# Performance work log

Hardware: AMD Instinct MI355X
Metric: run time of the kernel (lower is better)

## Reference

```python
import jax, jax.numpy as jnp
import numpy as np

N_NODES = 100000
N_EDGES = 600000
D_IN = 128
D_HID = 128
N_CLASSES = 64


def setup_inputs() -> dict:
    key = jax.random.key(0)
    ks = jax.random.split(key, 8)
    x = jax.random.normal(ks[0], (N_NODES, D_IN), dtype=jnp.float32)
    src = jax.random.randint(ks[1], (N_EDGES,), 0, N_NODES, dtype=jnp.int32)
    dst = jax.random.randint(ks[2], (N_EDGES,), 0, N_NODES, dtype=jnp.int32)
    s = 1.0 / np.sqrt(D_IN)
    W_self1 = jax.random.normal(ks[3], (D_IN, D_HID), dtype=jnp.float32) * s
    W_neigh1 = jax.random.normal(ks[4], (D_IN, D_HID), dtype=jnp.float32) * s
    b1 = jnp.zeros((D_HID,), dtype=jnp.float32)
    s2 = 1.0 / np.sqrt(D_HID)
    W_self2 = jax.random.normal(ks[5], (D_HID, N_CLASSES), dtype=jnp.float32) * s2
    W_neigh2 = jax.random.normal(ks[6], (D_HID, N_CLASSES), dtype=jnp.float32) * s2
    b2 = jnp.zeros((N_CLASSES,), dtype=jnp.float32)
    return {"x": x, "src": src, "dst": dst,
            "W_self1": W_self1, "W_neigh1": W_neigh1, "b1": b1,
            "W_self2": W_self2, "W_neigh2": W_neigh2, "b2": b2}


def _sage_conv(h, src, dst, W_self, W_neigh, b):
    # mean aggregation over in-neighbors (DGL SAGEConv 'mean')
    n = h.shape[0]
    nbr_sum = jax.ops.segment_sum(h[src], dst, num_segments=n)  # [N, d]
    deg = jax.ops.segment_sum(jnp.ones(src.shape, h.dtype), dst, num_segments=n)
    nbr_mean = nbr_sum / jnp.maximum(deg, 1.0)[:, None]
    return h @ W_self + nbr_mean @ W_neigh + b


def reference(x, src, dst, W_self1, W_neigh1, b1, W_self2, W_neigh2, b2):
    # dropout is identity in eval mode
    h = _sage_conv(x, src, dst, W_self1, W_neigh1, b1)
    h = jax.nn.relu(h)
    h = _sage_conv(h, src, dst, W_self2, W_neigh2, b2)
    return h
```

## Files before the change

### kernel.cpp

```cpp
#include <hip/hip_runtime.h>

#define N_NODES 100000
#define N_EDGES 600000
#define K_DIM 128
#define M2 64
#define NT_TILES ((N_NODES + 63) / 64)
#define GEMM_GRID 256

#define NBKT 800
#define NPB 125
#define HIST_BLOCKS 64
#define EPB (N_EDGES / HIST_BLOCKS)
#define BKT_CAP 1536

using frag_ab = __attribute__((ext_vector_type(8))) short;
using frag_cd = __attribute__((ext_vector_type(4))) float;

__device__ __forceinline__ unsigned short f2b(float f) {
  unsigned u = __builtin_bit_cast(unsigned, f);
  u = (u + 0x7fffu + ((u >> 16) & 1u)) >> 16;
  return (unsigned short)u;
}

__device__ __forceinline__ void gload_lds16(const void* gsrc, void* ldst) {
  __builtin_amdgcn_global_load_lds(
      (const __attribute__((address_space(1))) void*)gsrc,
      (__attribute__((address_space(3))) void*)ldst, 16, 0, 0);
}

__device__ __forceinline__ void lgkm_barrier() {
  __builtin_amdgcn_sched_barrier(0);
  asm volatile("s_waitcnt lgkmcnt(0)" ::: "memory");
  __builtin_amdgcn_s_barrier();
  __builtin_amdgcn_sched_barrier(0);
}

#define XB_BLOCKS ((N_NODES * K_DIM / 4 + 255) / 256)
#define W_ELEMS ((128 + 128 + 64 + 64) * 128)
#define WB_BLOCKS ((W_ELEMS + 255) / 256)
__global__ __launch_bounds__(256) void conv_all(const float* __restrict__ x,
                                                unsigned short* __restrict__ xb,
                                                const float* __restrict__ Ws1,
                                                const float* __restrict__ Wn1,
                                                const float* __restrict__ Ws2,
                                                const float* __restrict__ Wn2,
                                                unsigned short* __restrict__ Ws1T,
                                                unsigned short* __restrict__ Wn1T,
                                                unsigned short* __restrict__ Ws2T,
                                                unsigned short* __restrict__ Wn2T,
                                                const int* __restrict__ dst,
                                                int* __restrict__ pos,
                                                int* __restrict__ gbucket,
                                                int* __restrict__ base_tbl) {
  __shared__ int lcnt[NBKT];
  if (blockIdx.x < HIST_BLOCKS) {
    int tid = threadIdx.x;
    for (int i = tid; i < NBKT; i += 256) lcnt[i] = 0;
    __syncthreads();
    int e0 = blockIdx.x * EPB;
    for (int e = e0 + tid; e < e0 + EPB; e += 256) {
      int b = dst[e] / NPB;
      pos[e] = atomicAdd(&lcnt[b], 1);
    }
    __syncthreads();
    for (int i = tid; i < NBKT; i += 256) {
      int c = lcnt[i];
      if (c) base_tbl[blockIdx.x * NBKT + i] = atomicAdd(&gbucket[i], c);
    }
  } else if (blockIdx.x < HIST_BLOCKS + XB_BLOCKS) {
    long i = (long)(blockIdx.x - HIST_BLOCKS) * 256 + threadIdx.x;
    if (i >= (long)N_NODES * K_DIM / 4) return;
    float4 v = *(const float4*)(x + i * 4);
    ushort4 o;
    o.x = f2b(v.x); o.y = f2b(v.y); o.z = f2b(v.z); o.w = f2b(v.w);
    *(ushort4*)(xb + i * 4) = o;
  } else {
    int i = (blockIdx.x - HIST_BLOCKS - XB_BLOCKS) * 256 + threadIdx.x;
    if (i >= W_ELEMS) return;
    const float* W;
    unsigned short* WT;
    int M, li;
    if (i < 128 * 128)               { W = Ws1; WT = Ws1T; M = 128; li = i; }
    else if (i < 2 * 128 * 128)      { W = Wn1; WT = Wn1T; M = 128; li = i - 128 * 128; }
    else if (i < 2 * 128 * 128 + 64 * 128) { W = Ws2; WT = Ws2T; M = 64; li = i - 2 * 128 * 128; }
    else                             { W = Wn2; WT = Wn2T; M = 64; li = i - 2 * 128 * 128 - 64 * 128; }
    int n = li >> 7, k = li & 127;
    WT[li] = f2b(W[k * M + n]);
  }
}

__global__ __launch_bounds__(1024) void scan_buckets(const int* __restrict__ gbucket,
                                                     int* __restrict__ bucket_start,
                                                     int* __restrict__ row_ptr) {
  __shared__ int s[1024];
  int tid = threadIdx.x;
  int v = (tid < NBKT) ? gbucket[tid] : 0;
  s[tid] = v;
  __syncthreads();
  for (int off = 1; off < 1024; off <<= 1) {
    int t = (tid >= off) ? s[tid - off] : 0;
    __syncthreads();
    s[tid] += t;
    __syncthreads();
  }
  if (tid < NBKT) bucket_start[tid] = s[tid] - v;
  if (tid == 0) { bucket_start[NBKT] = N_EDGES; row_ptr[N_NODES] = N_EDGES; }
}

__global__ __launch_bounds__(256) void bucket_scatter(const int* __restrict__ src,
                                                      const int* __restrict__ dst,
                                                      const int* __restrict__ pos,
                                                      const int* __restrict__ bucket_start,
                                                      const int* __restrict__ base_tbl,
                                                      int* __restrict__ ebuf_src,
                                                      int* __restrict__ ebuf_ln) {
  int e = blockIdx.x * 256 + threadIdx.x;
  if (e >= N_EDGES) return;
  int d = dst[e];
  int b = d / NPB;
  int p = bucket_start[b] + base_tbl[(e / EPB) * NBKT + b] + pos[e];
  ebuf_src[p] = src[e];
  ebuf_ln[p] = d - b * NPB;
}

__global__ __launch_bounds__(512) void bucket_csr_agg1(const unsigned short* __restrict__ xb,
                                                       const int* __restrict__ ebuf_src,
                                                       const int* __restrict__ ebuf_ln,
                                                       const int* __restrict__ bucket_start,
                                                       int* __restrict__ row_ptr,
                                                       int* __restrict__ csr_src,
                                                       unsigned short* __restrict__ aggb) {
  __shared__ int cnt[128];
  __shared__ int sedge[BKT_CAP];
  int tid = threadIdx.x, b = blockIdx.x;
  int bs = bucket_start[b], be = bucket_start[b + 1];
  for (int i = tid; i < 128; i += 512) cnt[i] = 0;
  __syncthreads();

  int ln[3], lp[3], sv[3];
#pragma unroll
  for (int j = 0; j < 3; ++j) {
    int p = bs + tid + j * 512;
    if (p < be) {
      ln[j] = ebuf_ln[p];
      sv[j] = ebuf_src[p];
      lp[j] = atomicAdd(&cnt[ln[j]], 1);
    }
  }
  __syncthreads();
  for (int off = 1; off < 128; off <<= 1) {
    int t = 0;
    if (tid < 128 && tid >= off) t = cnt[tid - off];
    __syncthreads();
    if (tid < 128) cnt[tid] += t;
    __syncthreads();
  }
  for (int i = tid; i < NPB; i += 512)
    row_ptr[b * NPB + i] = bs + (i ? cnt[i - 1] : 0);
#pragma unroll
  for (int j = 0; j < 3; ++j) {
    int p = bs + tid + j * 512;
    if (p < be) {
      int l = ln[j];
      int loc = (l ? cnt[l - 1] : 0) + lp[j];
      sedge[loc] = sv[j];
      csr_src[bs + loc] = sv[j];
    }
  }
  __syncthreads();

  int nl = tid >> 4;
  int c = (tid & 15) << 3;
  for (int n0 = 0; n0 < NPB; n0 += 32) {
    int node = n0 + nl;
    if (node < NPB) {
      int beg = node ? cnt[node - 1] : 0;
      int end = cnt[node];
      float acc[8];
#pragma unroll
      for (int j = 0; j < 8; ++j) acc[j] = 0.f;
      for (int e0 = beg; e0 < end; e0 += 8) {
        int idx[8];
#pragma unroll
        for (int p = 0; p < 8; ++p) idx[p] = sedge[min(e0 + p, end - 1)];
        uint4 v[8];
#pragma unroll
        for (int p = 0; p < 8; ++p) v[p] = *(const uint4*)(xb + (size_t)idx[p] * K_DIM + c);
#pragma unroll
        for (int p = 0; p < 8; ++p) {
          float m = (e0 + p < end) ? 1.f : 0.f;
          unsigned u[4] = {v[p].x, v[p].y, v[p].z, v[p].w};
#pragma unroll
          for (int j = 0; j < 4; ++j) {
            acc[2 * j]     += m * __builtin_bit_cast(float, u[j] << 16);
            acc[2 * j + 1] += m * __builtin_bit_cast(float, u[j] & 0xffff0000u);
          }
        }
      }
      float inv = 1.0f / (float)max(end - beg, 1);
      uint4 o;
      unsigned* op = (unsigned*)&o;
#pragma unroll
      for (int j = 0; j < 4; ++j) {
        unsigned lo = f2b(acc[2 * j] * inv);
        unsigned hi = f2b(acc[2 * j + 1] * inv);
        op[j] = lo | (hi << 16);
      }
      *(uint4*)(aggb + (size_t)(b * NPB + node) * K_DIM + c) = o;
    }
  }
}

__global__ __launch_bounds__(256) void aggregate64_add(const unsigned short* __restrict__ g,
                                                       const int* __restrict__ row_ptr,
                                                       const int* __restrict__ csr_src,
                                                       float* __restrict__ out, int n) {
  int t = blockIdx.x * blockDim.x + threadIdx.x;
  int node = t >> 3;
  int c = (t & 7) << 3;
  if (node >= n) return;
  int beg = row_ptr[node], end = row_ptr[node + 1];
  float acc[8];
#pragma unroll
  for (int j = 0; j < 8; ++j) acc[j] = 0.f;

  if (end > beg) {
    for (int e0 = beg; e0 < end; e0 += 8) {
      int idx[8];
#pragma unroll
      for (int p = 0; p < 8; ++p) idx[p] = csr_src[min(e0 + p, end - 1)];
      uint4 v[8];
#pragma unroll
      for (int p = 0; p < 8; ++p) v[p] = *(const uint4*)(g + (size_t)idx[p] * M2 + c);
#pragma unroll
      for (int p = 0; p < 8; ++p) {
        float m = (e0 + p < end) ? 1.f : 0.f;
        unsigned u[4] = {v[p].x, v[p].y, v[p].z, v[p].w};
#pragma unroll
        for (int j = 0; j < 4; ++j) {
          acc[2 * j]     += m * __builtin_bit_cast(float, u[j] << 16);
          acc[2 * j + 1] += m * __builtin_bit_cast(float, u[j] & 0xffff0000u);
        }
      }
    }
  }
  float inv = 1.0f / (float)max(end - beg, 1);
  float* op = out + (size_t)node * M2 + c;
  float4 o0 = *(float4*)(op);
  float4 o1 = *(float4*)(op + 4);
  o0.x += acc[0] * inv; o0.y += acc[1] * inv; o0.z += acc[2] * inv; o0.w += acc[3] * inv;
  o1.x += acc[4] * inv; o1.y += acc[5] * inv; o1.z += acc[6] * inv; o1.w += acc[7] * inv;
  *(float4*)(op) = o0;
  *(float4*)(op + 4) = o1;
}

__device__ __forceinline__ void stage_tile(const unsigned short* xb, const unsigned short* aggb,
                                           int t, char* dstbase, int tid, int wave, int N) {
#pragma unroll
  for (int it = 0; it < 2; ++it) {
    int L = it * 8192 + tid * 16;
    int row = L >> 8;
    int srb = (L & 255) ^ ((row & 7) << 4);
    int node = t * 64 + row;
    if (node >= N) node = N - 1;
    char* d = dstbase + it * 8192 + wave * 1024;
    gload_lds16((const char*)xb + (size_t)node * 256 + srb, d);
    gload_lds16((const char*)aggb + (size_t)node * 256 + srb, d + 16384);
  }
}

__global__ __launch_bounds__(512, 2) void sage_fused_gemm(const unsigned short* __restrict__ xb,
                                                          const unsigned short* __restrict__ aggb,
                                                          const unsigned short* __restrict__ Ws1T,
                                                          const unsigned short* __restrict__ Wn1T,
                                                          const float* __restrict__ b1,
                                                          const unsigned short* __restrict__ Ws2T,
                                                          const unsigned short* __restrict__ Wn2T,
                                                          const float* __restrict__ b2,
                                                          float* __restrict__ out,
                                                          unsigned short* __restrict__ g, int N) {
  __shared__ char sL[163840];

  const int tid = threadIdx.x;
  const int wave = tid >> 6;
  const int lane = tid & 63;
  const int l15 = lane & 15;
  const int q = lane >> 4;
  const int nodeq = wave >> 1;
  const int fhalf = wave & 1;
  const int fbase = fhalf * 64;

#pragma unroll
  for (int it = 0; it < 4; ++it) {
    int L = it * 8192 + tid * 16;
    int row = L >> 8;
    int srb = (L & 255) ^ ((row & 7) << 4);
    char* d = sL + it * 8192 + wave * 1024;
    gload_lds16((const char*)Ws1T + row * 256 + srb, d);
    gload_lds16((const char*)Wn1T + row * 256 + srb, d + 32768);
  }
#pragma unroll
  for (int it = 0; it < 2; ++it) {
    int L = it * 8192 + tid * 16;
    int row = L >> 8;
    int srb = (L & 255) ^ ((row & 7) << 4);
    char* d = sL + 65536 + it * 8192 + wave * 1024;
    gload_lds16((const char*)Ws2T + row * 256 + srb, d);
    gload_lds16((const char*)Wn2T + row * 256 + srb, d + 16384);
  }
  int tt = blockIdx.x;
  if (tt < NT_TILES) stage_tile(xb, aggb, tt, sL + 98304, tid, wave, N);

  float4 bv1[4], bv2[4];
#pragma unroll
  for (int ft = 0; ft < 4; ++ft) {
    bv1[ft] = *(const float4*)(b1 + fbase + ft * 16 + q * 4);
    bv2[ft] = *(const float4*)(b2 + ft * 16 + q * 4);
  }

  int li = 0;
  for (; tt < NT_TILES; tt += GEMM_GRID, ++li) {
    char* cur = sL + 98304 + (li & 1) * 32768;
    char* nxt = sL + 98304 + ((li + 1) & 1) * 32768;

    __syncthreads();

    if (tt + GEMM_GRID < NT_TILES)
      stage_tile(xb, aggb, tt + GEMM_GRID, nxt, tid, wave, N);

    frag_cd acc[4];
#pragma unroll
    for (int ft = 0; ft < 4; ++ft) acc[ft] = (frag_cd)(0.f);

    const int xrow = nodeq * 16 + l15;
    const int xswz = (xrow & 7) << 4;
#pragma unroll
    for (int kb = 0; kb < 4; ++kb) {
      int base = kb * 64 + q * 16;
      frag_ab axk = *(const frag_ab*)(cur + xrow * 256 + (base ^ xswz));
      frag_ab agk = *(const frag_ab*)(cur + 16384 + xrow * 256 + (base ^ xswz));
      frag_ab fs[4], fn[4];
#pragma unroll
      for (int ft = 0; ft < 4; ++ft) {
        int wrow = fbase + ft * 16 + l15;
        int woff = base ^ ((wrow & 7) << 4);
        fs[ft] = *(const frag_ab*)(sL + wrow * 256 + woff);
        fn[ft] = *(const frag_ab*)(sL + 32768 + wrow * 256 + woff);
      }
#pragma unroll
      for (int ft = 0; ft < 4; ++ft) {
        acc[ft] = __builtin_amdgcn_mfma_f32_16x16x32_bf16(fs[ft], axk, acc[ft], 0, 0, 0);
        acc[ft] = __builtin_amdgcn_mfma_f32_16x16x32_bf16(fn[ft], agk, acc[ft], 0, 0, 0);
      }
    }

    lgkm_barrier();

#pragma unroll
    for (int ft = 0; ft < 4; ++ft) {
      int f0 = fbase + ft * 16 + q * 4;
      ushort4 o;
      o.x = f2b(fmaxf(acc[ft][0] + bv1[ft].x, 0.f));
      o.y = f2b(fmaxf(acc[ft][1] + bv1[ft].y, 0.f));
      o.z = f2b(fmaxf(acc[ft][2] + bv1[ft].z, 0.f));
      o.w = f2b(fmaxf(acc[ft][3] + bv1[ft].w, 0.f));
      *(ushort4*)(cur + xrow * 256 + ((f0 * 2) ^ xswz)) = o;
    }

    lgkm_barrier();

    const char* w2b = sL + 65536 + fhalf * 16384;
    frag_cd acc2[4];
#pragma unroll
    for (int ft = 0; ft < 4; ++ft) acc2[ft] = (frag_cd)(0.f);

#pragma unroll
    for (int kb = 0; kb < 4; ++kb) {
      int base = kb * 64 + q * 16;
      frag_ab ah = *(const frag_ab*)(cur + xrow * 256 + (base ^ xswz));
      frag_ab w2[4];
#pragma unroll
      for (int ft = 0; ft < 4; ++ft) {
        int wr = ft * 16 + l15;
        w2[ft] = *(const frag_ab*)(w2b + wr * 256 + (base ^ ((wr & 7) << 4)));
      }
#pragma unroll
      for (int ft = 0; ft < 4; ++ft)
        acc2[ft] = __builtin_amdgcn_mfma_f32_16x16x32_bf16(w2[ft], ah, acc2[ft], 0, 0, 0);
    }

    int node = tt * 64 + nodeq * 16 + l15;
    if (node < N) {
      if (fhalf == 0) {
#pragma unroll
        for (int ft = 0; ft < 4; ++ft) {
          int f0 = ft * 16 + q * 4;
          float4 o;
          o.x = acc2[ft][0] + bv2[ft].x;
          o.y = acc2[ft][1] + bv2[ft].y;
          o.z = acc2[ft][2] + bv2[ft].z;
          o.w = acc2[ft][3] + bv2[ft].w;
          *(float4*)(out + (size_t)node * M2 + f0) = o;
        }
      } else {
#pragma unroll
        for (int ft = 0; ft < 4; ++ft) {
          int f0 = ft * 16 + q * 4;
          ushort4 o;
          o.x = f2b(acc2[ft][0]);
          o.y = f2b(acc2[ft][1]);
          o.z = f2b(acc2[ft][2]);
          o.w = f2b(acc2[ft][3]);
          *(ushort4*)(g + (size_t)node * M2 + f0) = o;
        }
      }
    }
  }
}

extern "C" void kernel_launch(void* const* d_in, const int* in_sizes, int n_in,
                              void* d_out, int out_size, void* d_ws, size_t ws_size,
                              hipStream_t stream) {
  const float* x   = (const float*)d_in[0];
  const int*   src = (const int*)d_in[1];
  const int*   dst = (const int*)d_in[2];
  const float* Ws1 = (const float*)d_in[3];
  const float* Wn1 = (const float*)d_in[4];
  const float* b1  = (const float*)d_in[5];
  const float* Ws2 = (const float*)d_in[6];
  const float* Wn2 = (const float*)d_in[7];
  const float* b2  = (const float*)d_in[8];
  float* out = (float*)d_out;

  char* ws = (char*)d_ws;
  size_t off = 0;
  auto alloc = [&](size_t bytes) {
    void* p = ws + off;
    off = (off + bytes + 4095) & ~(size_t)4095;
    return p;
  };
  int* row_ptr      = (int*)alloc((size_t)(N_NODES + 1) * 4);
  int* pos          = (int*)alloc((size_t)N_EDGES * 4);
  int* gbucket      = (int*)alloc((size_t)NBKT * 4);
  int* bucket_start = (int*)alloc((size_t)(NBKT + 1) * 4);
  int* base_tbl     = (int*)alloc((size_t)HIST_BLOCKS * NBKT * 4);
  int* ebuf_src     = (int*)alloc((size_t)N_EDGES * 4);
  int* ebuf_ln      = (int*)alloc((size_t)N_EDGES * 4);
  int* csr_src      = (int*)alloc((size_t)N_EDGES * 4);
  unsigned short* xb   = (unsigned short*)alloc((size_t)N_NODES * K_DIM * 2);
  unsigned short* aggb = (unsigned short*)alloc((size_t)N_NODES * K_DIM * 2);
  unsigned short* g    = (unsigned short*)alloc((size_t)N_NODES * M2 * 2);
  unsigned short* Ws1T = (unsigned short*)alloc((size_t)128 * 128 * 2);
  unsigned short* Wn1T = (unsigned short*)alloc((size_t)128 * 128 * 2);
  unsigned short* Ws2T = (unsigned short*)alloc((size_t)64 * 128 * 2);
  unsigned short* Wn2T = (unsigned short*)alloc((size_t)64 * 128 * 2);

  hipMemsetAsync(gbucket, 0, (size_t)NBKT * 4, stream);

  conv_all<<<HIST_BLOCKS + XB_BLOCKS + WB_BLOCKS, 256, 0, stream>>>(
      x, xb, Ws1, Wn1, Ws2, Wn2, Ws1T, Wn1T, Ws2T, Wn2T, dst, pos, gbucket, base_tbl);

  scan_buckets<<<1, 1024, 0, stream>>>(gbucket, bucket_start, row_ptr);
  bucket_scatter<<<(N_EDGES + 255) / 256, 256, 0, stream>>>(
      src, dst, pos, bucket_start, base_tbl, ebuf_src, ebuf_ln);

  bucket_csr_agg1<<<NBKT, 512, 0, stream>>>(
      xb, ebuf_src, ebuf_ln, bucket_start, row_ptr, csr_src, aggb);

  sage_fused_gemm<<<GEMM_GRID, 512, 0, stream>>>(
      xb, aggb, Ws1T, Wn1T, b1, Ws2T, Wn2T, b2, out, g, N_NODES);

  {
    long t = (long)N_NODES * 8;
    aggregate64_add<<<(int)((t + 255) / 256), 256, 0, stream>>>(g, row_ptr, csr_src, out, N_NODES);
  }
}
```

Measured before the change: 211.6 us.

## Scatter edges into fixed-stride buckets inside histogram kernel, drop scan and scatter

The histogram blocks now do a second pass that writes each edge straight into a fixed-capacity bucket slot (stride 1024). Each edge is packed as a 20-bit source id plus a local node index in one int. This removes the bucket scan kernel, the separate scatter kernel and the pos/base_tbl intermediate arrays. The row pointers become a per-bucket table of 126 entries that the aggregation kernel indexes directly. In exchange it assumes no bucket exceeds 1024 edges and node ids fit in 20 bits, and it adds a second read of dst/src inside the histogram blocks.

```diff
diff --git a/kernel.cpp b/kernel.cpp
--- a/kernel.cpp
+++ b/kernel.cpp
@@ -11,7 +11,7 @@
 #define NPB 125
 #define HIST_BLOCKS 64
 #define EPB (N_EDGES / HIST_BLOCKS)
-#define BKT_CAP 1536
+#define BSTRIDE 1024
 
 using frag_ab = __attribute__((ext_vector_type(8))) short;
 using frag_cd = __attribute__((ext_vector_type(4))) float;
@@ -48,24 +48,31 @@
                                                 unsigned short* __restrict__ Wn1T,
                                                 unsigned short* __restrict__ Ws2T,
                                                 unsigned short* __restrict__ Wn2T,
+                                                const int* __restrict__ src,
                                                 const int* __restrict__ dst,
-                                                int* __restrict__ pos,
                                                 int* __restrict__ gbucket,
-                                                int* __restrict__ base_tbl) {
+                                                int* __restrict__ ebuf) {
   __shared__ int lcnt[NBKT];
+  __shared__ int lbase[NBKT];
   if (blockIdx.x < HIST_BLOCKS) {
     int tid = threadIdx.x;
     for (int i = tid; i < NBKT; i += 256) lcnt[i] = 0;
     __syncthreads();
     int e0 = blockIdx.x * EPB;
-    for (int e = e0 + tid; e < e0 + EPB; e += 256) {
-      int b = dst[e] / NPB;
-      pos[e] = atomicAdd(&lcnt[b], 1);
-    }
+    for (int e = e0 + tid; e < e0 + EPB; e += 256)
+      atomicAdd(&lcnt[dst[e] / NPB], 1);
     __syncthreads();
     for (int i = tid; i < NBKT; i += 256) {
       int c = lcnt[i];
-      if (c) base_tbl[blockIdx.x * NBKT + i] = atomicAdd(&gbucket[i], c);
+      lbase[i] = c ? atomicAdd(&gbucket[i], c) : 0;
+      lcnt[i] = 0;
+    }
+    __syncthreads();
+    for (int e = e0 + tid; e < e0 + EPB; e += 256) {
+      int d = dst[e];
+      int b = d / NPB;
+      int p = lbase[b] + atomicAdd(&lcnt[b], 1);
+      ebuf[b * BSTRIDE + p] = src[e] | ((d - b * NPB) << 20);
     }
   } else if (blockIdx.x < HIST_BLOCKS + XB_BLOCKS) {
     long i = (long)(blockIdx.x - HIST_BLOCKS) * 256 + threadIdx.x;
@@ -89,61 +96,28 @@
   }
 }
 
-__global__ __launch_bounds__(1024) void scan_buckets(const int* __restrict__ gbucket,
-                                                     int* __restrict__ bucket_start,
-                                                     int* __restrict__ row_ptr) {
-  __shared__ int s[1024];
-  int tid = threadIdx.x;
-  int v = (tid < NBKT) ? gbucket[tid] : 0;
-  s[tid] = v;
-  __syncthreads();
-  for (int off = 1; off < 1024; off <<= 1) {
-    int t = (tid >= off) ? s[tid - off] : 0;
-    __syncthreads();
-    s[tid] += t;
-    __syncthreads();
-  }
-  if (tid < NBKT) bucket_start[tid] = s[tid] - v;
-  if (tid == 0) { bucket_start[NBKT] = N_EDGES; row_ptr[N_NODES] = N_EDGES; }
-}
-
-__global__ __launch_bounds__(256) void bucket_scatter(const int* __restrict__ src,
-                                                      const int* __restrict__ dst,
-                                                      const int* __restrict__ pos,
-                                                      const int* __restrict__ bucket_start,
-                                                      const int* __restrict__ base_tbl,
-                                                      int* __restrict__ ebuf_src,
-                                                      int* __restrict__ ebuf_ln) {
-  int e = blockIdx.x * 256 + threadIdx.x;
-  if (e >= N_EDGES) return;
-  int d = dst[e];
-  int b = d / NPB;
-  int p = bucket_start[b] + base_tbl[(e / EPB) * NBKT + b] + pos[e];
-  ebuf_src[p] = src[e];
-  ebuf_ln[p] = d - b * NPB;
-}
-
 __global__ __launch_bounds__(512) void bucket_csr_agg1(const unsigned short* __restrict__ xb,
-                                                       const int* __restrict__ ebuf_src,
-                                                       const int* __restrict__ ebuf_ln,
-                                                       const int* __restrict__ bucket_start,
-                                                       int* __restrict__ row_ptr,
+                                                       const int* __restrict__ ebuf,
+                                                       const int* __restrict__ gbucket,
+                                                       int* __restrict__ rp,
                                                        int* __restrict__ csr_src,
                                                        unsigned short* __restrict__ aggb) {
   __shared__ int cnt[128];
-  __shared__ int sedge[BKT_CAP];
+  __shared__ int sedge[BSTRIDE];
   int tid = threadIdx.x, b = blockIdx.x;
-  int bs = bucket_start[b], be = bucket_start[b + 1];
+  int bs = b * BSTRIDE;
+  int ecnt = gbucket[b];
   for (int i = tid; i < 128; i += 512) cnt[i] = 0;
   __syncthreads();
 
-  int ln[3], lp[3], sv[3];
-#pragma unroll
-  for (int j = 0; j < 3; ++j) {
-    int p = bs + tid + j * 512;
-    if (p < be) {
-      ln[j] = ebuf_ln[p];
-      sv[j] = ebuf_src[p];
+  int ln[2], lp[2], sv[2];
+#pragma unroll
+  for (int j = 0; j < 2; ++j) {
+    int p = tid + j * 512;
+    if (p < ecnt) {
+      int pk = ebuf[bs + p];
+      sv[j] = pk & 0xFFFFF;
+      ln[j] = pk >> 20;
       lp[j] = atomicAdd(&cnt[ln[j]], 1);
     }
   }
@@ -155,12 +129,12 @@
     if (tid < 128) cnt[tid] += t;
     __syncthreads();
   }
-  for (int i = tid; i < NPB; i += 512)
-    row_ptr[b * NPB + i] = bs + (i ? cnt[i - 1] : 0);
-#pragma unroll
-  for (int j = 0; j < 3; ++j) {
-    int p = bs + tid + j * 512;
-    if (p < be) {
+  for (int i = tid; i < 126; i += 512)
+    rp[b * 126 + i] = bs + (i ? cnt[i - 1] : 0);
+#pragma unroll
+  for (int j = 0; j < 2; ++j) {
+    int p = tid + j * 512;
+    if (p < ecnt) {
       int l = ln[j];
       int loc = (l ? cnt[l - 1] : 0) + lp[j];
       sedge[loc] = sv[j];
@@ -212,14 +186,16 @@
 }
 
 __global__ __launch_bounds__(256) void aggregate64_add(const unsigned short* __restrict__ g,
-                                                       const int* __restrict__ row_ptr,
+                                                       const int* __restrict__ rp,
                                                        const int* __restrict__ csr_src,
                                                        float* __restrict__ out, int n) {
   int t = blockIdx.x * blockDim.x + threadIdx.x;
   int node = t >> 3;
   int c = (t & 7) << 3;
   if (node >= n) return;
-  int beg = row_ptr[node], end = row_ptr[node + 1];
+  int b = node / NPB;
+  int i = node - b * NPB;
+  int beg = rp[b * 126 + i], end = rp[b * 126 + i + 1];
   float acc[8];
 #pragma unroll
   for (int j = 0; j < 8; ++j) acc[j] = 0.f;
@@ -439,14 +415,10 @@
     off = (off + bytes + 4095) & ~(size_t)4095;
     return p;
   };
-  int* row_ptr      = (int*)alloc((size_t)(N_NODES + 1) * 4);
-  int* pos          = (int*)alloc((size_t)N_EDGES * 4);
-  int* gbucket      = (int*)alloc((size_t)NBKT * 4);
-  int* bucket_start = (int*)alloc((size_t)(NBKT + 1) * 4);
-  int* base_tbl     = (int*)alloc((size_t)HIST_BLOCKS * NBKT * 4);
-  int* ebuf_src     = (int*)alloc((size_t)N_EDGES * 4);
-  int* ebuf_ln      = (int*)alloc((size_t)N_EDGES * 4);
-  int* csr_src      = (int*)alloc((size_t)N_EDGES * 4);
+  int* gbucket  = (int*)alloc((size_t)NBKT * 4);
+  int* ebuf     = (int*)alloc((size_t)NBKT * BSTRIDE * 4);
+  int* rp       = (int*)alloc((size_t)NBKT * 126 * 4);
+  int* csr_src  = (int*)alloc((size_t)NBKT * BSTRIDE * 4);
   unsigned short* xb   = (unsigned short*)alloc((size_t)N_NODES * K_DIM * 2);
   unsigned short* aggb = (unsigned short*)alloc((size_t)N_NODES * K_DIM * 2);
   unsigned short* g    = (unsigned short*)alloc((size_t)N_NODES * M2 * 2);
@@ -458,20 +430,15 @@
   hipMemsetAsync(gbucket, 0, (size_t)NBKT * 4, stream);
 
   conv_all<<<HIST_BLOCKS + XB_BLOCKS + WB_BLOCKS, 256, 0, stream>>>(
-      x, xb, Ws1, Wn1, Ws2, Wn2, Ws1T, Wn1T, Ws2T, Wn2T, dst, pos, gbucket, base_tbl);
-
-  scan_buckets<<<1, 1024, 0, stream>>>(gbucket, bucket_start, row_ptr);
-  bucket_scatter<<<(N_EDGES + 255) / 256, 256, 0, stream>>>(
-      src, dst, pos, bucket_start, base_tbl, ebuf_src, ebuf_ln);
-
-  bucket_csr_agg1<<<NBKT, 512, 0, stream>>>(
-      xb, ebuf_src, ebuf_ln, bucket_start, row_ptr, csr_src, aggb);
+      x, xb, Ws1, Wn1, Ws2, Wn2, Ws1T, Wn1T, Ws2T, Wn2T, src, dst, gbucket, ebuf);
+
+  bucket_csr_agg1<<<NBKT, 512, 0, stream>>>(xb, ebuf, gbucket, rp, csr_src, aggb);
 
   sage_fused_gemm<<<GEMM_GRID, 512, 0, stream>>>(
       xb, aggb, Ws1T, Wn1T, b1, Ws2T, Wn2T, b2, out, g, N_NODES);
 
   {
     long t = (long)N_NODES * 8;
-    aggregate64_add<<<(int)((t + 255) / 256), 256, 0, stream>>>(g, row_ptr, csr_src, out, N_NODES);
-  }
-}
+    aggregate64_add<<<(int)((t + 255) / 256), 256, 0, stream>>>(g, rp, csr_src, out, N_NODES);
+  }
+}
```

After: 213.0 us. No clear change (+0.7%).
